# Kernel optimization log

Hardware: AMD Instinct MI355X
Metric: run time of the kernel (lower is better)

The kernel has to match this reference:

```python
import jax, jax.numpy as jnp
import numpy as np

NUM_HEADS = 16
D_MODEL = 1024
D_K = D_MODEL // NUM_HEADS
EPS = 1e-6


def setup_inputs() -> dict:
    key = jax.random.key(0)
    ks = jax.random.split(key, 12)
    B, S, D = 8, 1024, D_MODEL
    scale = 0.02
    return {
        "query": jax.random.normal(ks[0], (B, S, D), dtype=jnp.float32),
        "key": jax.random.normal(ks[1], (B, S, D), dtype=jnp.float32),
        "value": jax.random.normal(ks[2], (B, S, D), dtype=jnp.float32),
        "policy": jax.random.uniform(ks[3], (B, S, 1), dtype=jnp.float32),
        "wq_w": jax.random.normal(ks[4], (D, D), dtype=jnp.float32) * scale,
        "wq_b": jnp.zeros((D,), dtype=jnp.float32),
        "wk_w": jax.random.normal(ks[5], (D, D), dtype=jnp.float32) * scale,
        "wk_b": jnp.zeros((D,), dtype=jnp.float32),
        "wv_w": jax.random.normal(ks[6], (D, D), dtype=jnp.float32) * scale,
        "wv_b": jnp.zeros((D,), dtype=jnp.float32),
        "dense_w": jax.random.normal(ks[7], (D, D), dtype=jnp.float32) * scale,
        "dense_b": jnp.zeros((D,), dtype=jnp.float32),
    }


def _split_heads(x):
    B, S, D = x.shape
    return x.reshape(B, S, NUM_HEADS, D_K).transpose(0, 2, 1, 3)  # [B,H,S,dk]


def reference(query, key, value, policy, wq_w, wq_b, wk_w, wk_b, wv_w, wv_b, dense_w, dense_b):
    B, S, D = query.shape
    # torch Linear: y = x @ W.T + b
    q = _split_heads(query @ wq_w.T + wq_b)
    k = _split_heads(key @ wk_w.T + wk_b)
    v = _split_heads(value @ wv_w.T + wv_b)

    scores = jnp.einsum("bhqd,bhkd->bhqk", q, k) / jnp.sqrt(jnp.float32(D_K))
    # policy branch: exp * policy normalization (no softmax max-subtraction, faithful)
    attn_policy = policy.reshape(B, 1, 1, S)
    sc = jnp.exp(scores) * attn_policy
    p_attn = (sc + EPS / S) / (jnp.sum(sc, axis=-1, keepdims=True) + EPS)

    x = jnp.einsum("bhqk,bhkd->bhqd", p_attn, v)
    x = x.transpose(0, 2, 1, 3).reshape(B, S, D)
    out = x @ dense_w.T + dense_b  # dropout = identity (eval mode)
    return out
```

## Files before the change

kernel.cpp:

```cpp
#include <hip/hip_runtime.h>


#define Sdim 1024
#define Ddim 1024

typedef unsigned short u16;
typedef float f32x4 __attribute__((ext_vector_type(4)));
typedef float f32x16 __attribute__((ext_vector_type(16)));
typedef __bf16 bf16x8 __attribute__((ext_vector_type(8)));
typedef u16 u16x8 __attribute__((ext_vector_type(8)));
typedef __attribute__((address_space(3))) void lds_void;
typedef __attribute__((address_space(1))) void gbl_void;

__device__ __forceinline__ u16 f2bf(float f) {
    unsigned u = __float_as_uint(f);
    u += 0x7fffu + ((u >> 16) & 1u);
    return (u16)(u >> 16);
}
__device__ __forceinline__ void gld16(const void* g, void* l) {
    __builtin_amdgcn_global_load_lds((const gbl_void*)g, (lds_void*)l, 16, 0, 0);
}
__device__ __forceinline__ unsigned pk_bf16(float lo, float hi) {
    const unsigned ul = __float_as_uint(lo) + 0x8000u;
    const unsigned uh = __float_as_uint(hi) + 0x8000u;
    return __builtin_amdgcn_perm(uh, ul, 0x07060302u);
}
#define MFMA16(a, b, c) __builtin_amdgcn_mfma_f32_16x16x32_bf16((a), (b), (c), 0, 0, 0)
#define MFMA32(a, b, c) __builtin_amdgcn_mfma_f32_32x32x16_bf16((a), (b), (c), 0, 0, 0)

__global__ __launch_bounds__(256) void cvt_all(const float* __restrict__ s0,
                                               const float* __restrict__ s1,
                                               const float* __restrict__ s2,
                                               const float* __restrict__ s3,
                                               const float* __restrict__ s4,
                                               const float* __restrict__ s5,
                                               const float* __restrict__ s6,
                                               u16* __restrict__ d0, u16* __restrict__ d1,
                                               u16* __restrict__ d2, u16* __restrict__ d3,
                                               u16* __restrict__ d4, u16* __restrict__ d5,
                                               u16* __restrict__ d6) {
    const int z = blockIdx.y;
    if (z >= 3 && blockIdx.x >= 512) return;
    const float* s = z == 0 ? s0 : z == 1 ? s1 : z == 2 ? s2 : z == 3 ? s3
                   : z == 4 ? s4 : z == 5 ? s5 : s6;
    u16* d = z == 0 ? d0 : z == 1 ? d1 : z == 2 ? d2 : z == 3 ? d3
           : z == 4 ? d4 : z == 5 ? d5 : d6;
    const float sc = (z == 3) ? 0.125f : 1.0f;
    const int i = (blockIdx.x * 256 + threadIdx.x) * 8;
    const float4 a = *(const float4*)(s + i);
    const float4 b = *(const float4*)(s + i + 4);
    u16x8 o;
    o[0] = f2bf(a.x * sc); o[1] = f2bf(a.y * sc); o[2] = f2bf(a.z * sc); o[3] = f2bf(a.w * sc);
    o[4] = f2bf(b.x * sc); o[5] = f2bf(b.y * sc); o[6] = f2bf(b.z * sc); o[7] = f2bf(b.w * sc);
    *(u16x8*)(d + i) = o;
}

template <bool OUT_BF16>
__device__ __forceinline__ void gemm_body(const u16* __restrict__ A,
                                          const u16* __restrict__ W,
                                          const float* __restrict__ bias, float bscale,
                                          void* __restrict__ Cout,
                                          u16* As, u16* Bs,
                                          int m0, int n0) {
    const int tid  = threadIdx.x;
    const int wave = tid >> 6;
    const int lane = tid & 63;
    const int l15  = lane & 15;
    const int quad = lane >> 4;
    const int wm = (wave >> 1) * 64;
    const int wn = (wave & 1) * 64;

    const int e0 = wave * 512 + lane * 8;
    const int r0 = e0 >> 5, c0 = e0 & 31;
    const int e1 = 2048 + e0;
    const int r1 = e1 >> 5, c1 = e1 & 31;
    const u16* Ag0 = A + (size_t)(m0 + r0) * Ddim + c0;
    const u16* Ag1 = A + (size_t)(m0 + r1) * Ddim + c1;
    const u16* Wg0 = W + (size_t)(n0 + r0) * Ddim + c0;
    const u16* Wg1 = W + (size_t)(n0 + r1) * Ddim + c1;
    u16* As0 = As + wave * 512;
    u16* As1 = As + 2048 + wave * 512;
    u16* Bs0 = Bs + wave * 512;
    u16* Bs1 = Bs + 2048 + wave * 512;

    f32x4 acc[4][4] = {};

    for (int k0 = 0; k0 < Ddim; k0 += 32) {
        __syncthreads();
        gld16(Ag0 + k0, As0);
        gld16(Ag1 + k0, As1);
        gld16(Wg0 + k0, Bs0);
        gld16(Wg1 + k0, Bs1);
        __syncthreads();
        bf16x8 af[4], bfr[4];
#pragma unroll
        for (int i = 0; i < 4; ++i)
            af[i] = *(const bf16x8*)(As + (wm + i * 16 + l15) * 32 + quad * 8);
#pragma unroll
        for (int j = 0; j < 4; ++j)
            bfr[j] = *(const bf16x8*)(Bs + (wn + j * 16 + l15) * 32 + quad * 8);
#pragma unroll
        for (int i = 0; i < 4; ++i)
#pragma unroll
            for (int j = 0; j < 4; ++j)
                acc[i][j] = MFMA16(af[i], bfr[j], acc[i][j]);
    }

    float bv[4];
#pragma unroll
    for (int j = 0; j < 4; ++j) bv[j] = bias[n0 + wn + j * 16 + l15] * bscale;
#pragma unroll
    for (int i = 0; i < 4; ++i)
#pragma unroll
        for (int j = 0; j < 4; ++j)
#pragma unroll
            for (int r = 0; r < 4; ++r) {
                const int row = m0 + wm + i * 16 + quad * 4 + r;
                const int col = n0 + wn + j * 16 + l15;
                const float v = acc[i][j][r] + bv[j];
                if (OUT_BF16)
                    ((u16*)Cout)[(size_t)row * Ddim + col] = f2bf(v);
                else
                    ((float*)Cout)[(size_t)row * Ddim + col] = v;
            }
}

__global__ __launch_bounds__(256) void gemm_qkv(const u16* __restrict__ A0, const u16* __restrict__ A1,
                                                const u16* __restrict__ A2,
                                                const u16* __restrict__ W0, const u16* __restrict__ W1,
                                                const u16* __restrict__ W2,
                                                const float* __restrict__ b0, const float* __restrict__ b1,
                                                const float* __restrict__ b2,
                                                u16* __restrict__ C0, u16* __restrict__ C1,
                                                u16* __restrict__ C2) {
    __shared__ __align__(16) u16 As[128 * 32];
    __shared__ __align__(16) u16 Bs[128 * 32];
    const int z = blockIdx.z;
    const u16* A = z == 0 ? A0 : z == 1 ? A1 : A2;
    const u16* W = z == 0 ? W0 : z == 1 ? W1 : W2;
    const float* bias = z == 0 ? b0 : z == 1 ? b1 : b2;
    u16* C = z == 0 ? C0 : z == 1 ? C1 : C2;
    const float bsc = (z == 0) ? 0.125f : 1.0f;
    gemm_body<true>(A, W, bias, bsc, (void*)C, As, Bs, blockIdx.x * 128, blockIdx.y * 128);
}

__global__ __launch_bounds__(256) void gemm_dense(const u16* __restrict__ A,
                                                  const u16* __restrict__ W,
                                                  const float* __restrict__ bias,
                                                  float* __restrict__ C) {
    __shared__ __align__(16) u16 As[128 * 32];
    __shared__ __align__(16) u16 Bs[128 * 32];
    gemm_body<false>(A, W, bias, 1.0f, (void*)C, As, Bs, blockIdx.x * 128, blockIdx.y * 128);
}

__global__ __launch_bounds__(256) void transp_v(const u16* __restrict__ Vp,
                                                u16* __restrict__ Vt) {
    __shared__ __align__(16) u16 Ts[64][72];
    const int bh = blockIdx.x, s0 = blockIdx.y * 64;
    const int b = bh >> 4, h = bh & 15;
    const int tid = threadIdx.x;
#pragma unroll
    for (int p = 0; p < 2; ++p) {
        const int e = p * 2048 + tid * 8;
        const int r = e >> 6, c = e & 63;
        *(u16x8*)&Ts[r][c] =
            *(const u16x8*)(Vp + ((size_t)(b * Sdim + s0 + r)) * Ddim + h * 64 + c);
    }
    __syncthreads();
    const int d = tid >> 2, sp = tid & 3;
#pragma unroll
    for (int g = 0; g < 2; ++g) {
        u16x8 o;
#pragma unroll
        for (int j = 0; j < 8; ++j) o[j] = Ts[sp * 16 + g * 8 + j][d];
        *(u16x8*)(Vt + ((size_t)(bh * 64 + d)) * Sdim + s0 + sp * 16 + g * 8) = o;
    }
}

__global__ __launch_bounds__(256, 2) void attn_mfma(const u16* __restrict__ Qp,
                                                    const u16* __restrict__ Kp,
                                                    const u16* __restrict__ Vt,
                                                    const float* __restrict__ pol,
                                                    u16* __restrict__ Xb) {
    __shared__ __align__(16) u16 lds[28288];
    u16* Qs = lds;
    u16* Ks = lds + 18432;
    u16* Vs = lds + 23040;
    float* pols = (float*)(lds + 27648);
    float* denb = pols + 64;

    const int tid  = threadIdx.x;
    const int w    = tid >> 6;
    const int lane = tid & 63;
    const int l31  = lane & 31;
    const unsigned hsel = lane >> 5;
    const int q0 = blockIdx.x * 256;
    const int bh = blockIdx.y;
    const size_t bS = (size_t)(bh >> 4) * Sdim;
    const int col0 = (bh & 15) * 64;
    const int sr = tid >> 2;
    const int sc4 = tid & 3;

#pragma unroll
    for (int rg = 0; rg < 4; ++rg) {
        const int r = rg * 64 + sr;
#pragma unroll
        for (int g = 0; g < 2; ++g) {
            const int ch = sc4 + g * 4;
            *(u16x8*)(Qs + r * 72 + ch * 8) =
                *(const u16x8*)(Qp + (bS + q0 + r) * Ddim + col0 + ch * 8);
        }
    }
    __syncthreads();
    bf16x8 Qf[2][4];
#pragma unroll
    for (int qt = 0; qt < 2; ++qt)
#pragma unroll
        for (int dkt = 0; dkt < 4; ++dkt)
            Qf[qt][dkt] = *(const bf16x8*)(Qs + (w * 64 + qt * 32 + l31) * 72 +
                                           dkt * 16 + hsel * 8);

    f32x16 X[2][2] = {};
    float den[2] = {0.f, 0.f};

    for (int kt = 0; kt < 16; ++kt) {
        const int kbase = kt * 64;
        __syncthreads();
#pragma unroll
        for (int g = 0; g < 2; ++g) {
            const int ch = sc4 + g * 4;
            *(u16x8*)(Ks + sr * 72 + ch * 8) =
                *(const u16x8*)(Kp + (bS + kbase + sr) * Ddim + col0 + ch * 8);
            *(u16x8*)(Vs + sr * 72 + ch * 8) =
                *(const u16x8*)(Vt + ((size_t)(bh * 64 + sr)) * Sdim + kbase + ch * 8);
        }
        if (tid < 64) pols[tid] = pol[bS + kbase + tid];
        __syncthreads();

#pragma unroll
        for (int t32 = 0; t32 < 2; ++t32) {
            float polv[16];
#pragma unroll
            for (int e = 0; e < 16; ++e)
                polv[e] = pols[t32 * 32 + (e & 3) + 8 * (e >> 2) + 4 * hsel];
            bf16x8 Kf[4];
#pragma unroll
            for (int dkt = 0; dkt < 4; ++dkt)
                Kf[dkt] = *(const bf16x8*)(Ks + (t32 * 32 + l31) * 72 +
                                           dkt * 16 + hsel * 8);
#pragma unroll
            for (int qt = 0; qt < 2; ++qt) {
                f32x16 S = {};
#pragma unroll
                for (int dkt = 0; dkt < 4; ++dkt)
                    S = MFMA32(Kf[dkt], Qf[qt][dkt], S);
                float p[16];
#pragma unroll
                for (int e = 0; e < 16; ++e) {
                    p[e] = __expf(S[e]) * polv[e];
                    den[qt] += p[e];
                }
                unsigned pk_[8], sw[8];
#pragma unroll
                for (int g = 0; g < 4; ++g) {
                    pk_[2 * g]     = pk_bf16(p[4 * g + 0], p[4 * g + 1]);
                    pk_[2 * g + 1] = pk_bf16(p[4 * g + 2], p[4 * g + 3]);
                }
#pragma unroll
                for (int i = 0; i < 8; ++i)
                    sw[i] = (unsigned)__shfl_xor((int)pk_[i], 32);
#pragma unroll
                for (int tau = 0; tau < 2; ++tau) {
                    union { unsigned u[4]; bf16x8 v; } Af;
                    Af.u[0] = hsel ? sw[(2 * tau + 1) * 2 + 0] : pk_[(2 * tau) * 2 + 0];
                    Af.u[1] = hsel ? sw[(2 * tau + 1) * 2 + 1] : pk_[(2 * tau) * 2 + 1];
                    Af.u[2] = hsel ? pk_[(2 * tau + 1) * 2 + 0] : sw[(2 * tau) * 2 + 0];
                    Af.u[3] = hsel ? pk_[(2 * tau + 1) * 2 + 1] : sw[(2 * tau) * 2 + 1];
#pragma unroll
                    for (int ndt = 0; ndt < 2; ++ndt) {
                        const bf16x8 Vf =
                            *(const bf16x8*)(Vs + (ndt * 32 + l31) * 72 +
                                             t32 * 32 + tau * 16 + hsel * 8);
                        X[qt][ndt] = MFMA32(Af.v, Vf, X[qt][ndt]);
                    }
                }
            }
        }
    }

#pragma unroll
    for (int qt = 0; qt < 2; ++qt) {
        den[qt] += __shfl_xor(den[qt], 32);
        denb[w * 64 + qt * 32 + l31] = 1.0f / (den[qt] + 1e-6f);
    }
    u16* Xout = Qs;
#pragma unroll
    for (int qt = 0; qt < 2; ++qt) {
        float invv[16];
#pragma unroll
        for (int e = 0; e < 16; ++e)
            invv[e] = denb[w * 64 + qt * 32 + (e & 3) + 8 * (e >> 2) + 4 * hsel];
#pragma unroll
        for (int ndt = 0; ndt < 2; ++ndt)
#pragma unroll
            for (int e = 0; e < 16; ++e) {
                const int rho = (e & 3) + 8 * (e >> 2) + 4 * hsel;
                Xout[(w * 64 + qt * 32 + rho) * 72 + ndt * 32 + l31] =
                    f2bf(X[qt][ndt][e] * invv[e]);
            }
    }
    __syncthreads();
#pragma unroll
    for (int rg = 0; rg < 4; ++rg) {
        const int r = rg * 64 + sr;
#pragma unroll
        for (int g = 0; g < 2; ++g) {
            const int ch = sc4 + g * 4;
            *(u16x8*)(Xb + (bS + q0 + r) * Ddim + col0 + ch * 8) =
                *(const u16x8*)(Xout + r * 72 + ch * 8);
        }
    }
}

extern "C" void kernel_launch(void* const* d_in, const int* in_sizes, int n_in,
                              void* d_out, int out_size, void* d_ws, size_t ws_size,
                              hipStream_t stream) {
    const float* query   = (const float*)d_in[0];
    const float* key     = (const float*)d_in[1];
    const float* value   = (const float*)d_in[2];
    const float* policy  = (const float*)d_in[3];
    const float* wq_w    = (const float*)d_in[4];
    const float* wq_b    = (const float*)d_in[5];
    const float* wk_w    = (const float*)d_in[6];
    const float* wk_b    = (const float*)d_in[7];
    const float* wv_w    = (const float*)d_in[8];
    const float* wv_b    = (const float*)d_in[9];
    const float* dense_w = (const float*)d_in[10];
    const float* dense_b = (const float*)d_in[11];

    const size_t MM = 1u << 20;
    const size_t A8 = 8 * MM;
    u16* qa  = (u16*)d_ws;
    u16* ka  = qa + A8;
    u16* va  = ka + A8;
    u16* wqb = va + A8;
    u16* wkb = wqb + MM;
    u16* wvb = wkb + MM;
    u16* wdb = wvb + MM;
    u16* Qp  = wdb + MM;
    u16* Kp  = Qp + A8;
    u16* Vp  = Kp + A8;
    u16* Vtg = ka;
    u16* Xb  = qa;

    cvt_all<<<dim3(4096, 7), 256, 0, stream>>>(query, key, value, wq_w, wk_w, wv_w, dense_w,
                                               qa, ka, va, wqb, wkb, wvb, wdb);

    gemm_qkv<<<dim3(64, 8, 3), 256, 0, stream>>>(qa, ka, va, wqb, wkb, wvb,
                                                 wq_b, wk_b, wv_b, Qp, Kp, Vp);
    transp_v<<<dim3(128, 16), 256, 0, stream>>>(Vp, Vtg);

    attn_mfma<<<dim3(4, 128), 256, 0, stream>>>(Qp, Kp, Vtg, policy, Xb);

    gemm_dense<<<dim3(64, 8), 256, 0, stream>>>(Xb, wdb, dense_b, (float*)d_out);
}
```

Baseline: 314.1 us.

## Replace GEMMs with 256x256-tile 8-wave double-buffered swizzled kernel

Both the QKV projection and the dense output GEMM move from a 128x128 tile with 4 waves and K-step 32, synchronised twice per step, to a 256x256 tile with 8 waves and K-step 64. The new kernel double-buffers the tiles in 128KB of XOR-swizzled LDS, interleaves the prefetch of the next tile with four MFMA phases using explicit vmcnt waits, barriers and setprio, and remaps block indices so that neighbouring blocks share tiles in cache. The aim is higher arithmetic intensity, overlap of loads with compute, and fewer LDS bank conflicts. In exchange it uses many more registers and much more LDS, launches only 384 and 128 blocks, and depends on hand-tuned wait counts being correct.

```diff
diff --git a/kernel.cpp b/kernel.cpp
--- a/kernel.cpp
+++ b/kernel.cpp
@@ -27,6 +27,11 @@
 }
 #define MFMA16(a, b, c) __builtin_amdgcn_mfma_f32_16x16x32_bf16((a), (b), (c), 0, 0, 0)
 #define MFMA32(a, b, c) __builtin_amdgcn_mfma_f32_32x32x16_bf16((a), (b), (c), 0, 0, 0)
+
+#define WAITVM(n) asm volatile("s_waitcnt vmcnt(" #n ")" ::: "memory")
+#define WAITLGKM0 asm volatile("s_waitcnt lgkmcnt(0)" ::: "memory")
+#define SBAR() __builtin_amdgcn_s_barrier()
+#define SCHEDB() __builtin_amdgcn_sched_barrier(0)
 
 __global__ __launch_bounds__(256) void cvt_all(const float* __restrict__ s0,
                                                const float* __restrict__ s1,
@@ -55,69 +60,150 @@
     *(u16x8*)(d + i) = o;
 }
 
+__device__ __forceinline__ void mfma_block(f32x4 (&acc)[8][4], const bf16x8 (&Af)[4][2],
+                                           const bf16x8 (&Bf)[2][2], int mb, int nb) {
+#pragma unroll
+    for (int mi = 0; mi < 4; ++mi)
+#pragma unroll
+        for (int ni = 0; ni < 2; ++ni) {
+            f32x4 c = acc[mb + mi][nb + ni];
+            c = MFMA16(Af[mi][0], Bf[ni][0], c);
+            c = MFMA16(Af[mi][1], Bf[ni][1], c);
+            acc[mb + mi][nb + ni] = c;
+        }
+}
+
 template <bool OUT_BF16>
-__device__ __forceinline__ void gemm_body(const u16* __restrict__ A,
-                                          const u16* __restrict__ W,
-                                          const float* __restrict__ bias, float bscale,
-                                          void* __restrict__ Cout,
-                                          u16* As, u16* Bs,
-                                          int m0, int n0) {
+__device__ __forceinline__ void gemm8_body(const u16* __restrict__ A,
+                                           const u16* __restrict__ W,
+                                           const float* __restrict__ bias, float bscale,
+                                           void* __restrict__ Cout,
+                                           char* __restrict__ smem,
+                                           int m0, int n0) {
     const int tid  = threadIdx.x;
-    const int wave = tid >> 6;
+    const int w    = tid >> 6;
     const int lane = tid & 63;
     const int l15  = lane & 15;
     const int quad = lane >> 4;
-    const int wm = (wave >> 1) * 64;
-    const int wn = (wave & 1) * 64;
-
-    const int e0 = wave * 512 + lane * 8;
-    const int r0 = e0 >> 5, c0 = e0 & 31;
-    const int e1 = 2048 + e0;
-    const int r1 = e1 >> 5, c1 = e1 & 31;
-    const u16* Ag0 = A + (size_t)(m0 + r0) * Ddim + c0;
-    const u16* Ag1 = A + (size_t)(m0 + r1) * Ddim + c1;
-    const u16* Wg0 = W + (size_t)(n0 + r0) * Ddim + c0;
-    const u16* Wg1 = W + (size_t)(n0 + r1) * Ddim + c1;
-    u16* As0 = As + wave * 512;
-    u16* As1 = As + 2048 + wave * 512;
-    u16* Bs0 = Bs + wave * 512;
-    u16* Bs1 = Bs + 2048 + wave * 512;
-
-    f32x4 acc[4][4] = {};
-
-    for (int k0 = 0; k0 < Ddim; k0 += 32) {
-        __syncthreads();
-        gld16(Ag0 + k0, As0);
-        gld16(Ag1 + k0, As1);
-        gld16(Wg0 + k0, Bs0);
-        gld16(Wg1 + k0, Bs1);
-        __syncthreads();
-        bf16x8 af[4], bfr[4];
-#pragma unroll
-        for (int i = 0; i < 4; ++i)
-            af[i] = *(const bf16x8*)(As + (wm + i * 16 + l15) * 32 + quad * 8);
-#pragma unroll
-        for (int j = 0; j < 4; ++j)
-            bfr[j] = *(const bf16x8*)(Bs + (wn + j * 16 + l15) * 32 + quad * 8);
-#pragma unroll
-        for (int i = 0; i < 4; ++i)
-#pragma unroll
-            for (int j = 0; j < 4; ++j)
-                acc[i][j] = MFMA16(af[i], bfr[j], acc[i][j]);
-    }
+    const int wr   = w >> 2;
+    const int wc   = w & 3;
+
+    const int srA = w * 8 + (lane >> 3);
+    const int srB = (w & 3) * 8 + (w >> 2) * 64 + (lane >> 3);
+    const int scol = (((lane & 7) ^ ((lane >> 3) & 7)) << 3);
+    const u16* pa = A + (size_t)(m0 + srA) * Ddim + scol;
+    const u16* pb = W + (size_t)(n0 + srB) * Ddim + scol;
+    char* sA = smem + w * 1024;
+    char* sB = smem + 65536 + (w & 3) * 1024 + (w >> 2) * 8192;
+
+#define STG_A(h, kk, b)                                                          \
+    do {                                                                         \
+        gld16(pa + (size_t)(h) * 65536 + (kk) * 64,                              \
+              sA + (b) * 32768 + (h) * 8192);                                    \
+        gld16(pa + (size_t)(h) * 65536 + 131072 + (kk) * 64,                     \
+              sA + (b) * 32768 + (h) * 8192 + 16384);                            \
+    } while (0)
+#define STG_B(h, kk, b)                                                          \
+    do {                                                                         \
+        gld16(pb + (size_t)(h) * 32768 + (kk) * 64,                              \
+              sB + (b) * 32768 + (h) * 4096);                                    \
+        gld16(pb + (size_t)(h) * 32768 + 131072 + (kk) * 64,                     \
+              sB + (b) * 32768 + (h) * 4096 + 16384);                            \
+    } while (0)
+
+    const char* Ab = smem + (size_t)(wr * 128 + l15) * 128;
+    const char* Bb = smem + 65536 + (size_t)(wc * 64 + l15) * 128;
+    const int cx = ((quad ^ (l15 & 7)) << 4);
+
+    f32x4 acc[8][4] = {};
+    bf16x8 Af[4][2], Bf0[2][2], Bf1[2][2];
+
+    STG_A(0, 0, 0);
+    STG_B(0, 0, 0);
+    STG_B(1, 0, 0);
+    STG_A(1, 0, 0);
+    WAITVM(4);
+    SBAR();
+
+    for (int t = 0; t < 16; ++t) {
+        const int bo = (t & 1) * 32768;
+        const int nb = 1 - (t & 1);
+        const bool pf = (t < 15);
+#pragma unroll
+        for (int mi = 0; mi < 4; ++mi) {
+            Af[mi][0] = *(const bf16x8*)(Ab + bo + mi * 2048 + cx);
+            Af[mi][1] = *(const bf16x8*)(Ab + bo + mi * 2048 + (cx ^ 64));
+        }
+#pragma unroll
+        for (int ni = 0; ni < 2; ++ni) {
+            Bf0[ni][0] = *(const bf16x8*)(Bb + bo + ni * 2048 + cx);
+            Bf0[ni][1] = *(const bf16x8*)(Bb + bo + ni * 2048 + (cx ^ 64));
+        }
+        if (pf) STG_A(0, t + 1, nb);
+        SCHEDB();
+        if (pf) { WAITVM(4); } else { WAITVM(2); }
+        SBAR();
+        WAITLGKM0;
+        SCHEDB();
+        __builtin_amdgcn_s_setprio(1);
+        mfma_block(acc, Af, Bf0, 0, 0);
+        __builtin_amdgcn_s_setprio(0);
+        SBAR();
+#pragma unroll
+        for (int ni = 0; ni < 2; ++ni) {
+            Bf1[ni][0] = *(const bf16x8*)(Bb + bo + (2 + ni) * 2048 + cx);
+            Bf1[ni][1] = *(const bf16x8*)(Bb + bo + (2 + ni) * 2048 + (cx ^ 64));
+        }
+        if (pf) STG_B(0, t + 1, nb);
+        SCHEDB();
+        if (pf) { WAITVM(4); } else { WAITVM(0); }
+        SBAR();
+        WAITLGKM0;
+        SCHEDB();
+        __builtin_amdgcn_s_setprio(1);
+        mfma_block(acc, Af, Bf1, 0, 2);
+        __builtin_amdgcn_s_setprio(0);
+        SBAR();
+#pragma unroll
+        for (int mi = 0; mi < 4; ++mi) {
+            Af[mi][0] = *(const bf16x8*)(Ab + bo + (4 + mi) * 2048 + cx);
+            Af[mi][1] = *(const bf16x8*)(Ab + bo + (4 + mi) * 2048 + (cx ^ 64));
+        }
+        if (pf) STG_B(1, t + 1, nb);
+        SCHEDB();
+        SBAR();
+        WAITLGKM0;
+        SCHEDB();
+        __builtin_amdgcn_s_setprio(1);
+        mfma_block(acc, Af, Bf0, 4, 0);
+        __builtin_amdgcn_s_setprio(0);
+        SBAR();
+        if (pf) STG_A(1, t + 1, nb);
+        SCHEDB();
+        if (pf) { WAITVM(4); }
+        SBAR();
+        SCHEDB();
+        __builtin_amdgcn_s_setprio(1);
+        mfma_block(acc, Af, Bf1, 4, 2);
+        __builtin_amdgcn_s_setprio(0);
+        SBAR();
+    }
+#undef STG_A
+#undef STG_B
 
     float bv[4];
 #pragma unroll
-    for (int j = 0; j < 4; ++j) bv[j] = bias[n0 + wn + j * 16 + l15] * bscale;
-#pragma unroll
-    for (int i = 0; i < 4; ++i)
-#pragma unroll
-        for (int j = 0; j < 4; ++j)
+    for (int ni = 0; ni < 4; ++ni)
+        bv[ni] = bias[n0 + wc * 64 + ni * 16 + l15] * bscale;
+#pragma unroll
+    for (int mi = 0; mi < 8; ++mi)
+#pragma unroll
+        for (int ni = 0; ni < 4; ++ni)
 #pragma unroll
             for (int r = 0; r < 4; ++r) {
-                const int row = m0 + wm + i * 16 + quad * 4 + r;
-                const int col = n0 + wn + j * 16 + l15;
-                const float v = acc[i][j][r] + bv[j];
+                const int row = m0 + wr * 128 + mi * 16 + quad * 4 + r;
+                const int col = n0 + wc * 64 + ni * 16 + l15;
+                const float v = acc[mi][ni][r] + bv[ni];
                 if (OUT_BF16)
                     ((u16*)Cout)[(size_t)row * Ddim + col] = f2bf(v);
                 else
@@ -125,32 +211,34 @@
             }
 }
 
-__global__ __launch_bounds__(256) void gemm_qkv(const u16* __restrict__ A0, const u16* __restrict__ A1,
-                                                const u16* __restrict__ A2,
-                                                const u16* __restrict__ W0, const u16* __restrict__ W1,
-                                                const u16* __restrict__ W2,
-                                                const float* __restrict__ b0, const float* __restrict__ b1,
-                                                const float* __restrict__ b2,
-                                                u16* __restrict__ C0, u16* __restrict__ C1,
-                                                u16* __restrict__ C2) {
-    __shared__ __align__(16) u16 As[128 * 32];
-    __shared__ __align__(16) u16 Bs[128 * 32];
-    const int z = blockIdx.z;
+__global__ __launch_bounds__(512, 2) void gemm8_qkv(
+        const u16* __restrict__ A0, const u16* __restrict__ A1, const u16* __restrict__ A2,
+        const u16* __restrict__ W0, const u16* __restrict__ W1, const u16* __restrict__ W2,
+        const float* __restrict__ b0, const float* __restrict__ b1, const float* __restrict__ b2,
+        u16* __restrict__ C0, u16* __restrict__ C1, u16* __restrict__ C2) {
+    __shared__ __align__(16) char smem[131072];
+    const int d = blockIdx.x + (blockIdx.y << 2) + (blockIdx.z << 7);
+    const int s = (d & 7) * 48 + (d >> 3);
+    const int z = s >> 7;
+    const int rr = s & 127;
+    const int tm = rr >> 2, tn = rr & 3;
     const u16* A = z == 0 ? A0 : z == 1 ? A1 : A2;
     const u16* W = z == 0 ? W0 : z == 1 ? W1 : W2;
     const float* bias = z == 0 ? b0 : z == 1 ? b1 : b2;
     u16* C = z == 0 ? C0 : z == 1 ? C1 : C2;
     const float bsc = (z == 0) ? 0.125f : 1.0f;
-    gemm_body<true>(A, W, bias, bsc, (void*)C, As, Bs, blockIdx.x * 128, blockIdx.y * 128);
-}
-
-__global__ __launch_bounds__(256) void gemm_dense(const u16* __restrict__ A,
-                                                  const u16* __restrict__ W,
-                                                  const float* __restrict__ bias,
-                                                  float* __restrict__ C) {
-    __shared__ __align__(16) u16 As[128 * 32];
-    __shared__ __align__(16) u16 Bs[128 * 32];
-    gemm_body<false>(A, W, bias, 1.0f, (void*)C, As, Bs, blockIdx.x * 128, blockIdx.y * 128);
+    gemm8_body<true>(A, W, bias, bsc, (void*)C, smem, tm * 256, tn * 256);
+}
+
+__global__ __launch_bounds__(512, 2) void gemm8_dense(const u16* __restrict__ A,
+                                                      const u16* __restrict__ W,
+                                                      const float* __restrict__ bias,
+                                                      float* __restrict__ C) {
+    __shared__ __align__(16) char smem[131072];
+    const int d = blockIdx.x + (blockIdx.y << 2);
+    const int s = (d & 7) * 16 + (d >> 3);
+    const int tm = s >> 2, tn = s & 3;
+    gemm8_body<false>(A, W, bias, 1.0f, (void*)C, smem, tm * 256, tn * 256);
 }
 
 __global__ __launch_bounds__(256) void transp_v(const u16* __restrict__ Vp,
@@ -356,11 +444,11 @@
     cvt_all<<<dim3(4096, 7), 256, 0, stream>>>(query, key, value, wq_w, wk_w, wv_w, dense_w,
                                                qa, ka, va, wqb, wkb, wvb, wdb);
 
-    gemm_qkv<<<dim3(64, 8, 3), 256, 0, stream>>>(qa, ka, va, wqb, wkb, wvb,
-                                                 wq_b, wk_b, wv_b, Qp, Kp, Vp);
+    gemm8_qkv<<<dim3(4, 32, 3), 512, 0, stream>>>(qa, ka, va, wqb, wkb, wvb,
+                                                  wq_b, wk_b, wv_b, Qp, Kp, Vp);
     transp_v<<<dim3(128, 16), 256, 0, stream>>>(Vp, Vtg);
 
     attn_mfma<<<dim3(4, 128), 256, 0, stream>>>(Qp, Kp, Vtg, policy, Xb);
 
-    gemm_dense<<<dim3(64, 8), 256, 0, stream>>>(Xb, wdb, dense_b, (float*)d_out);
-}
+    gemm8_dense<<<dim3(4, 32), 512, 0, stream>>>(Xb, wdb, dense_b, (float*)d_out);
+}
```

New measurement: 306.5 us. 2.4% less time.

## Rewrite projection GEMMs with double-buffered 256x128 tiles, swizzled LDS, block remap

Applied to the files above, without the earlier changes.

Replaces the single-buffered 128x128, k=32 GEMM with a 512-thread, 256x128-tile kernel. It uses k=64 stages, double-buffers the global-to-LDS loads so the next tile is prefetched while MFMAs run on the current one, and XOR-swizzles the LDS layout to avoid bank conflicts. Blocks are linearized and remapped so consecutive blocks spread across XCDs. The aim is to hide load latency and halve the syncs per k-step, at the cost of 96KB of LDS per block, which limits occupancy.

```diff
diff --git a/kernel.cpp b/kernel.cpp
--- a/kernel.cpp
+++ b/kernel.cpp
@@ -27,6 +27,7 @@
 }
 #define MFMA16(a, b, c) __builtin_amdgcn_mfma_f32_16x16x32_bf16((a), (b), (c), 0, 0, 0)
 #define MFMA32(a, b, c) __builtin_amdgcn_mfma_f32_32x32x16_bf16((a), (b), (c), 0, 0, 0)
+#define SCHEDB() __builtin_amdgcn_sched_barrier(0)
 
 __global__ __launch_bounds__(256) void cvt_all(const float* __restrict__ s0,
                                                const float* __restrict__ s1,
@@ -56,67 +57,84 @@
 }
 
 template <bool OUT_BF16>
-__device__ __forceinline__ void gemm_body(const u16* __restrict__ A,
-                                          const u16* __restrict__ W,
-                                          const float* __restrict__ bias, float bscale,
-                                          void* __restrict__ Cout,
-                                          u16* As, u16* Bs,
-                                          int m0, int n0) {
+__device__ __forceinline__ void gemm2p_body(const u16* __restrict__ A,
+                                            const u16* __restrict__ W,
+                                            const float* __restrict__ bias, float bscale,
+                                            void* __restrict__ Cout,
+                                            char* __restrict__ smem,
+                                            int m0, int n0) {
     const int tid  = threadIdx.x;
-    const int wave = tid >> 6;
+    const int w    = tid >> 6;
     const int lane = tid & 63;
     const int l15  = lane & 15;
     const int quad = lane >> 4;
-    const int wm = (wave >> 1) * 64;
-    const int wn = (wave & 1) * 64;
-
-    const int e0 = wave * 512 + lane * 8;
-    const int r0 = e0 >> 5, c0 = e0 & 31;
-    const int e1 = 2048 + e0;
-    const int r1 = e1 >> 5, c1 = e1 & 31;
-    const u16* Ag0 = A + (size_t)(m0 + r0) * Ddim + c0;
-    const u16* Ag1 = A + (size_t)(m0 + r1) * Ddim + c1;
-    const u16* Wg0 = W + (size_t)(n0 + r0) * Ddim + c0;
-    const u16* Wg1 = W + (size_t)(n0 + r1) * Ddim + c1;
-    u16* As0 = As + wave * 512;
-    u16* As1 = As + 2048 + wave * 512;
-    u16* Bs0 = Bs + wave * 512;
-    u16* Bs1 = Bs + 2048 + wave * 512;
+    const int wr   = w >> 1;
+    const int wc   = w & 1;
+
+    const int lrow = lane >> 3;
+    const int scol = (((lane & 7) ^ lrow) << 3);
+    const u16* pa = A + (size_t)(m0 + w * 32 + lrow) * Ddim + scol;
+    const u16* pb = W + (size_t)(n0 + w * 16 + lrow) * Ddim + scol;
+    char* sAw = smem + w * 4096;
+    char* sBw = smem + 65536 + w * 2048;
+
+#define STG(t, b)                                                             \
+    do {                                                                      \
+        const int k0 = (t) * 64;                                              \
+        gld16(pa + k0,             sAw + (b) * 32768);                        \
+        gld16(pa + k0 + 8 * 1024,  sAw + (b) * 32768 + 1024);                 \
+        gld16(pa + k0 + 16 * 1024, sAw + (b) * 32768 + 2048);                 \
+        gld16(pa + k0 + 24 * 1024, sAw + (b) * 32768 + 3072);                 \
+        gld16(pb + k0,             sBw + (b) * 16384);                        \
+        gld16(pb + k0 + 8 * 1024,  sBw + (b) * 16384 + 1024);                 \
+    } while (0)
+
+    const char* Ab = smem + (size_t)(wr * 64 + l15) * 128;
+    const char* Bb = smem + 65536 + (size_t)(wc * 64 + l15) * 128;
+    const int cx = ((quad ^ (l15 & 7)) << 4);
 
     f32x4 acc[4][4] = {};
 
-    for (int k0 = 0; k0 < Ddim; k0 += 32) {
+    STG(0, 0);
+    __syncthreads();
+
+    for (int t = 0; t < 16; ++t) {
+        const int boA = (t & 1) * 32768;
+        const int boB = (t & 1) * 16384;
+        if (t < 15) STG(t + 1, (t & 1) ^ 1);
+        SCHEDB();
+#pragma unroll
+        for (int ks = 0; ks < 2; ++ks) {
+            const int cxs = cx ^ (ks << 6);
+            bf16x8 af[4], bfr[4];
+#pragma unroll
+            for (int i = 0; i < 4; ++i)
+                af[i] = *(const bf16x8*)(Ab + boA + i * 2048 + cxs);
+#pragma unroll
+            for (int j = 0; j < 4; ++j)
+                bfr[j] = *(const bf16x8*)(Bb + boB + j * 2048 + cxs);
+#pragma unroll
+            for (int i = 0; i < 4; ++i)
+#pragma unroll
+                for (int j = 0; j < 4; ++j)
+                    acc[i][j] = MFMA16(af[i], bfr[j], acc[i][j]);
+        }
         __syncthreads();
-        gld16(Ag0 + k0, As0);
-        gld16(Ag1 + k0, As1);
-        gld16(Wg0 + k0, Bs0);
-        gld16(Wg1 + k0, Bs1);
-        __syncthreads();
-        bf16x8 af[4], bfr[4];
-#pragma unroll
-        for (int i = 0; i < 4; ++i)
-            af[i] = *(const bf16x8*)(As + (wm + i * 16 + l15) * 32 + quad * 8);
+    }
+#undef STG
+
+    float bv[4];
+#pragma unroll
+    for (int j = 0; j < 4; ++j)
+        bv[j] = bias[n0 + wc * 64 + j * 16 + l15] * bscale;
+#pragma unroll
+    for (int i = 0; i < 4; ++i)
 #pragma unroll
         for (int j = 0; j < 4; ++j)
-            bfr[j] = *(const bf16x8*)(Bs + (wn + j * 16 + l15) * 32 + quad * 8);
-#pragma unroll
-        for (int i = 0; i < 4; ++i)
-#pragma unroll
-            for (int j = 0; j < 4; ++j)
-                acc[i][j] = MFMA16(af[i], bfr[j], acc[i][j]);
-    }
-
-    float bv[4];
-#pragma unroll
-    for (int j = 0; j < 4; ++j) bv[j] = bias[n0 + wn + j * 16 + l15] * bscale;
-#pragma unroll
-    for (int i = 0; i < 4; ++i)
-#pragma unroll
-        for (int j = 0; j < 4; ++j)
 #pragma unroll
             for (int r = 0; r < 4; ++r) {
-                const int row = m0 + wm + i * 16 + quad * 4 + r;
-                const int col = n0 + wn + j * 16 + l15;
+                const int row = m0 + wr * 64 + i * 16 + quad * 4 + r;
+                const int col = n0 + wc * 64 + j * 16 + l15;
                 const float v = acc[i][j][r] + bv[j];
                 if (OUT_BF16)
                     ((u16*)Cout)[(size_t)row * Ddim + col] = f2bf(v);
@@ -125,32 +143,34 @@
             }
 }
 
-__global__ __launch_bounds__(256) void gemm_qkv(const u16* __restrict__ A0, const u16* __restrict__ A1,
-                                                const u16* __restrict__ A2,
-                                                const u16* __restrict__ W0, const u16* __restrict__ W1,
-                                                const u16* __restrict__ W2,
-                                                const float* __restrict__ b0, const float* __restrict__ b1,
-                                                const float* __restrict__ b2,
-                                                u16* __restrict__ C0, u16* __restrict__ C1,
-                                                u16* __restrict__ C2) {
-    __shared__ __align__(16) u16 As[128 * 32];
-    __shared__ __align__(16) u16 Bs[128 * 32];
-    const int z = blockIdx.z;
+__global__ __launch_bounds__(512, 2) void gemm2p_qkv(
+        const u16* __restrict__ A0, const u16* __restrict__ A1, const u16* __restrict__ A2,
+        const u16* __restrict__ W0, const u16* __restrict__ W1, const u16* __restrict__ W2,
+        const float* __restrict__ b0, const float* __restrict__ b1, const float* __restrict__ b2,
+        u16* __restrict__ C0, u16* __restrict__ C1, u16* __restrict__ C2) {
+    __shared__ __align__(16) char smem[98304];
+    const int d = blockIdx.x;
+    const int s = (d & 7) * 96 + (d >> 3);
+    const int z = s >> 8;
+    const int rr = s & 255;
+    const int tm = rr >> 3, tn = rr & 7;
     const u16* A = z == 0 ? A0 : z == 1 ? A1 : A2;
     const u16* W = z == 0 ? W0 : z == 1 ? W1 : W2;
     const float* bias = z == 0 ? b0 : z == 1 ? b1 : b2;
     u16* C = z == 0 ? C0 : z == 1 ? C1 : C2;
     const float bsc = (z == 0) ? 0.125f : 1.0f;
-    gemm_body<true>(A, W, bias, bsc, (void*)C, As, Bs, blockIdx.x * 128, blockIdx.y * 128);
-}
-
-__global__ __launch_bounds__(256) void gemm_dense(const u16* __restrict__ A,
-                                                  const u16* __restrict__ W,
-                                                  const float* __restrict__ bias,
-                                                  float* __restrict__ C) {
-    __shared__ __align__(16) u16 As[128 * 32];
-    __shared__ __align__(16) u16 Bs[128 * 32];
-    gemm_body<false>(A, W, bias, 1.0f, (void*)C, As, Bs, blockIdx.x * 128, blockIdx.y * 128);
+    gemm2p_body<true>(A, W, bias, bsc, (void*)C, smem, tm * 256, tn * 128);
+}
+
+__global__ __launch_bounds__(512, 2) void gemm2p_dense(const u16* __restrict__ A,
+                                                       const u16* __restrict__ W,
+                                                       const float* __restrict__ bias,
+                                                       float* __restrict__ C) {
+    __shared__ __align__(16) char smem[98304];
+    const int d = blockIdx.x;
+    const int s = (d & 7) * 32 + (d >> 3);
+    const int tm = s >> 3, tn = s & 7;
+    gemm2p_body<false>(A, W, bias, 1.0f, (void*)C, smem, tm * 256, tn * 128);
 }
 
 __global__ __launch_bounds__(256) void transp_v(const u16* __restrict__ Vp,
@@ -356,11 +376,11 @@
     cvt_all<<<dim3(4096, 7), 256, 0, stream>>>(query, key, value, wq_w, wk_w, wv_w, dense_w,
                                                qa, ka, va, wqb, wkb, wvb, wdb);
 
-    gemm_qkv<<<dim3(64, 8, 3), 256, 0, stream>>>(qa, ka, va, wqb, wkb, wvb,
-                                                 wq_b, wk_b, wv_b, Qp, Kp, Vp);
+    gemm2p_qkv<<<dim3(768), 512, 0, stream>>>(qa, ka, va, wqb, wkb, wvb,
+                                              wq_b, wk_b, wv_b, Qp, Kp, Vp);
     transp_v<<<dim3(128, 16), 256, 0, stream>>>(Vp, Vtg);
 
     attn_mfma<<<dim3(4, 128), 256, 0, stream>>>(Qp, Kp, Vtg, policy, Xb);
 
-    gemm_dense<<<dim3(64, 8), 256, 0, stream>>>(Xb, wdb, dense_b, (float*)d_out);
-}
+    gemm2p_dense<<<dim3(256), 512, 0, stream>>>(Xb, wdb, dense_b, (float*)d_out);
+}
```

New measurement: 298.7 us. 4.9% less time.
